# Performance work log

Hardware: AMD Instinct MI355X
Metric: run time of the kernel (lower is better)

## Reference

```python
import jax, jax.numpy as jnp
import numpy as np

N = 100000
E = 1600000
IN_C = 128
OUT_C = 64
ALPHA = 0.2  # LeakyReLU negative slope


def _xavier(key, shape, gain=1.414):
    fan_in, fan_out = shape[-2] if len(shape) > 1 else shape[-1], shape[-1]
    bound = gain * np.sqrt(6.0 / (shape[0] * 0 + (shape[-2] if len(shape) > 1 else 1) + shape[-1])) if False else gain * np.sqrt(6.0 / (sum(shape)))
    return jax.random.uniform(key, shape, jnp.float32, -bound, bound)


def setup_inputs() -> dict:
    key = jax.random.key(0)
    k_x, k_s, k_o, k_w, k_a = jax.random.split(key, 5)
    x = jax.random.normal(k_x, (N, IN_C), jnp.float32)
    # edge list with no self-loops (so remove_self_loops is a no-op)
    src = jax.random.randint(k_s, (E,), 0, N)
    off = jax.random.randint(k_o, (E,), 1, N)
    dst = (src + off) % N
    edge_index = jnp.stack([src, dst]).astype(jnp.int64)
    W = _xavier(k_w, (IN_C, OUT_C))
    a = _xavier(k_a, (1, 2 * OUT_C))
    return {"x": x, "W": W, "a": a, "edge_index": edge_index}


def reference(x, W, a, edge_index):
    h = x @ W                               # [N, D]
    n, d = h.shape
    loops = jnp.arange(n, dtype=edge_index.dtype)
    src = jnp.concatenate([edge_index[0], loops])   # add_self_loops
    dst = jnp.concatenate([edge_index[1], loops])
    # (cat(h[src], h[dst]) * a).sum(-1) == h[src]@a1 + h[dst]@a2
    a1, a2 = a[0, :d], a[0, d:]
    s = h @ a1                              # [N]
    t = h @ a2                              # [N]
    edge_e = jnp.exp(jax.nn.leaky_relu(s[src] + t[dst], negative_slope=ALPHA))  # [E+N]
    e_expsum = jax.ops.segment_sum(edge_e, src, num_segments=n)                  # [N]
    h_prime = jax.ops.segment_sum(edge_e[:, None] * h[dst], src, num_segments=n)  # [N, D]
    return h_prime / e_expsum[:, None]
```

## Files before the change

### kernel.cpp

```cpp
#include <hip/hip_runtime.h>
#include <math.h>

#define IN_C 128
#define OUT_C 64
#define ALPHA 0.2f

#define SCAN_BLOCK 256
#define SCAN_ITEMS 4
#define SCAN_TILE (SCAN_BLOCK * SCAN_ITEMS)

#define LDK 136

#define PA_EPT 16
#define PA_TILE (256 * PA_EPT)
#define BSH 9
#define NPB 512
#define MAXB 256

typedef __attribute__((ext_vector_type(8))) short short8;
typedef __attribute__((ext_vector_type(4))) float v4f;

__device__ __forceinline__ ushort f2b(float f) {
  unsigned u = __float_as_uint(f);
  u += 0x7fffu + ((u >> 16) & 1u);
  return (ushort)(u >> 16);
}
__device__ __forceinline__ float b2f(ushort h) {
  return __uint_as_float(((unsigned)h) << 16);
}

__global__ __launch_bounds__(256) void gemm_st_kernel(
    const float* __restrict__ x, const float* __restrict__ W,
    const float* __restrict__ a, ushort* __restrict__ hb,
    float* __restrict__ s, float* __restrict__ t, int n_nodes, int n_tiles) {
  __shared__ ushort xs[64 * LDK];
  __shared__ ushort ws[64 * LDK];

  const int tid = threadIdx.x;
  const int wave = tid >> 6;
  const int lane = tid & 63;
  const int li = lane & 15;
  const int quad = lane >> 4;

  for (int i = tid; i < IN_C * OUT_C; i += 256) {
    const int k = i >> 6;
    const int n = i & 63;
    ws[n * LDK + k] = f2b(W[i]);
  }
  __syncthreads();

  short8 bfrag[4][4];
#pragma unroll
  for (int ct = 0; ct < 4; ++ct)
#pragma unroll
    for (int kk = 0; kk < 4; ++kk)
      bfrag[ct][kk] =
          *(const short8*)&ws[(ct * 16 + li) * LDK + kk * 32 + quad * 8];

  float a1v[4], a2v[4];
#pragma unroll
  for (int ct = 0; ct < 4; ++ct) {
    a1v[ct] = a[ct * 16 + li];
    a2v[ct] = a[OUT_C + ct * 16 + li];
  }

  for (int tile = blockIdx.x; tile < n_tiles; tile += gridDim.x) {
    const int row0 = tile * 64;

    __syncthreads();
    for (int i = tid; i < 64 * (IN_C / 4); i += 256) {
      const int r = i >> 5;
      const int c4 = i & 31;
      int row = row0 + r;
      row = row < n_nodes ? row : n_nodes - 1;
      const float4 v = *(const float4*)&x[(size_t)row * IN_C + c4 * 4];
      uint2 p;
      p.x = (unsigned)f2b(v.x) | ((unsigned)f2b(v.y) << 16);
      p.y = (unsigned)f2b(v.z) | ((unsigned)f2b(v.w) << 16);
      *(uint2*)&xs[r * LDK + c4 * 4] = p;
    }
    __syncthreads();

    v4f acc[4];
#pragma unroll
    for (int ct = 0; ct < 4; ++ct) acc[ct] = (v4f){0.f, 0.f, 0.f, 0.f};

    const int rbase = wave * 16;
#pragma unroll
    for (int kk = 0; kk < 4; ++kk) {
      const short8 af =
          *(const short8*)&xs[(rbase + li) * LDK + kk * 32 + quad * 8];
#pragma unroll
      for (int ct = 0; ct < 4; ++ct)
        acc[ct] = __builtin_amdgcn_mfma_f32_16x16x32_bf16(af, bfrag[ct][kk],
                                                          acc[ct], 0, 0, 0);
    }

    const int growbase = row0 + rbase + quad * 4;
    float ps[4] = {0.f, 0.f, 0.f, 0.f};
    float pt[4] = {0.f, 0.f, 0.f, 0.f};
#pragma unroll
    for (int ct = 0; ct < 4; ++ct) {
#pragma unroll
      for (int r = 0; r < 4; ++r) {
        const float hv = acc[ct][r];
        ps[r] += hv * a1v[ct];
        pt[r] += hv * a2v[ct];
        const int grow = growbase + r;
        if (grow < n_nodes)
          hb[(size_t)grow * OUT_C + ct * 16 + li] = f2b(hv);
      }
    }
#pragma unroll
    for (int m = 1; m <= 8; m <<= 1) {
#pragma unroll
      for (int r = 0; r < 4; ++r) {
        ps[r] += __shfl_xor(ps[r], m, 64);
        pt[r] += __shfl_xor(pt[r], m, 64);
      }
    }
    if (li < 4) {
      const int grow = growbase + li;
      if (grow < n_nodes) {
        const float sv = li == 0 ? ps[0] : li == 1 ? ps[1] : li == 2 ? ps[2] : ps[3];
        const float tv = li == 0 ? pt[0] : li == 1 ? pt[1] : li == 2 ? pt[2] : pt[3];
        s[grow] = sv;
        t[grow] = tv;
      }
    }
  }
}

__global__ __launch_bounds__(256) void pa_count(const int* __restrict__ src,
                                                int* __restrict__ counts_tbl,
                                                int nblk_a, int E) {
  __shared__ int hist[MAXB];
  const int tid = threadIdx.x;
  hist[tid] = 0;
  __syncthreads();
  const int e0 = blockIdx.x * PA_TILE + tid * PA_EPT;
  if (e0 + PA_EPT <= E) {
#pragma unroll
    for (int i = 0; i < PA_EPT / 4; ++i) {
      const int4 v = *(const int4*)(src + e0 + i * 4);
      atomicAdd(&hist[v.x >> BSH], 1);
      atomicAdd(&hist[v.y >> BSH], 1);
      atomicAdd(&hist[v.z >> BSH], 1);
      atomicAdd(&hist[v.w >> BSH], 1);
    }
  } else {
    for (int e = e0; e < E; ++e) atomicAdd(&hist[src[e] >> BSH], 1);
  }
  __syncthreads();
  counts_tbl[(size_t)tid * nblk_a + blockIdx.x] = hist[tid];
}

__global__ __launch_bounds__(SCAN_BLOCK) void scan_partial(
    const int* __restrict__ cnt, int* __restrict__ block_sums, int n) {
  const int tid = threadIdx.x;
  const int base = blockIdx.x * SCAN_TILE + tid * SCAN_ITEMS;
  int s = 0;
#pragma unroll
  for (int i = 0; i < SCAN_ITEMS; ++i) {
    const int idx = base + i;
    if (idx < n) s += cnt[idx];
  }
  __shared__ int wsum[SCAN_BLOCK / 64];
#pragma unroll
  for (int off = 32; off; off >>= 1) s += __shfl_down(s, off, 64);
  if ((tid & 63) == 0) wsum[tid >> 6] = s;
  __syncthreads();
  if (tid == 0) {
    int tot = 0;
#pragma unroll
    for (int w = 0; w < SCAN_BLOCK / 64; ++w) tot += wsum[w];
    block_sums[blockIdx.x] = tot;
  }
}

__global__ __launch_bounds__(1024) void scan_blocksums(
    int* __restrict__ block_sums, int nb) {
  __shared__ int sh[1024];
  const int tid = threadIdx.x;
  const int v = (tid < nb) ? block_sums[tid] : 0;
  sh[tid] = v;
  __syncthreads();
  int val = v;
  for (int off = 1; off < 1024; off <<= 1) {
    const int other = (tid >= off) ? sh[tid - off] : 0;
    __syncthreads();
    val += other;
    sh[tid] = val;
    __syncthreads();
  }
  if (tid < nb) block_sums[tid] = val - v;
}

__global__ __launch_bounds__(SCAN_BLOCK) void scan_final_plain(
    const int* __restrict__ cnt, const int* __restrict__ block_sums,
    int* __restrict__ outv, int n) {
  __shared__ int tsum[SCAN_BLOCK];
  const int tid = threadIdx.x;
  const int base = blockIdx.x * SCAN_TILE + tid * SCAN_ITEMS;
  int local[SCAN_ITEMS];
  int s = 0;
#pragma unroll
  for (int i = 0; i < SCAN_ITEMS; ++i) {
    const int idx = base + i;
    local[i] = (idx < n) ? cnt[idx] : 0;
    s += local[i];
  }
  tsum[tid] = s;
  __syncthreads();
  int val = s;
  for (int off = 1; off < SCAN_BLOCK; off <<= 1) {
    const int other = (tid >= off) ? tsum[tid - off] : 0;
    __syncthreads();
    val += other;
    tsum[tid] = val;
    __syncthreads();
  }
  int prefix = block_sums[blockIdx.x] + (val - s);
#pragma unroll
  for (int i = 0; i < SCAN_ITEMS; ++i) {
    const int idx = base + i;
    if (idx < n) {
      outv[idx] = prefix;
      prefix += local[i];
    }
  }
}

__global__ __launch_bounds__(256) void pa_scatter(
    const int* __restrict__ src, const int* __restrict__ dst,
    const int* __restrict__ bases_tbl, int2* __restrict__ bpair, int nblk_a,
    int nbuck, int E) {
  __shared__ int cur[MAXB];
  const int tid = threadIdx.x;
  cur[tid] = (tid < nbuck) ? bases_tbl[(size_t)tid * nblk_a + blockIdx.x] : 0;
  __syncthreads();
  const int e0 = blockIdx.x * PA_TILE + tid * PA_EPT;
  if (e0 + PA_EPT <= E) {
#pragma unroll
    for (int i = 0; i < PA_EPT / 4; ++i) {
      const int4 sv = *(const int4*)(src + e0 + i * 4);
      const int4 dv = *(const int4*)(dst + e0 + i * 4);
      const int p0 = atomicAdd(&cur[sv.x >> BSH], 1);
      const int p1 = atomicAdd(&cur[sv.y >> BSH], 1);
      const int p2 = atomicAdd(&cur[sv.z >> BSH], 1);
      const int p3 = atomicAdd(&cur[sv.w >> BSH], 1);
      bpair[p0] = make_int2(sv.x, dv.x);
      bpair[p1] = make_int2(sv.y, dv.y);
      bpair[p2] = make_int2(sv.z, dv.z);
      bpair[p3] = make_int2(sv.w, dv.w);
    }
  } else {
    for (int e = e0; e < E; ++e) {
      const int sv = src[e];
      const int dv = dst[e];
      const int p = atomicAdd(&cur[sv >> BSH], 1);
      bpair[p] = make_int2(sv, dv);
    }
  }
}

__global__ __launch_bounds__(256) void pb_build(
    const int2* __restrict__ bpair, const int* __restrict__ bases_tbl,
    int* __restrict__ offs, int* __restrict__ dst_sorted, int n_nodes,
    int nblk_a, int nbuck, int E) {
  __shared__ int cnt[NPB];
  __shared__ int loffs[NPB];
  __shared__ int tsum[256];
  const int b = blockIdx.x;
  const int tid = threadIdx.x;
  const int bstart = bases_tbl[(size_t)b * nblk_a];
  const int bend = (b + 1 < nbuck) ? bases_tbl[(size_t)(b + 1) * nblk_a] : E;
  const int nbase = b << BSH;

  for (int i = tid; i < NPB; i += 256) cnt[i] = 0;
  __syncthreads();
  for (int e = bstart + tid; e < bend; e += 256)
    atomicAdd(&cnt[bpair[e].x - nbase], 1);
  __syncthreads();

  const int a0 = cnt[2 * tid];
  const int a1 = cnt[2 * tid + 1];
  const int tv = a0 + a1;
  tsum[tid] = tv;
  __syncthreads();
  int val = tv;
  for (int off = 1; off < 256; off <<= 1) {
    const int other = (tid >= off) ? tsum[tid - off] : 0;
    __syncthreads();
    val += other;
    tsum[tid] = val;
    __syncthreads();
  }
  const int pfx = val - tv;
  loffs[2 * tid] = pfx;
  loffs[2 * tid + 1] = pfx + a0;
  __syncthreads();

  for (int i = tid; i < NPB; i += 256) {
    const int node = nbase + i;
    const int gpos = bstart + loffs[i];
    if (node < n_nodes) offs[node] = gpos;
    cnt[i] = gpos;
  }
  if (b == 0 && tid == 0) offs[n_nodes] = E;
  __syncthreads();

  for (int e = bstart + tid; e < bend; e += 256) {
    const int2 pr = bpair[e];
    const int pos = atomicAdd(&cnt[pr.x - nbase], 1);
    dst_sorted[pos] = pr.y;
  }
}

__global__ __launch_bounds__(256) void aggregate_kernel(
    const int* __restrict__ offs, const int* __restrict__ dst_sorted,
    const uint* __restrict__ hbp, const float* __restrict__ s,
    const float* __restrict__ t, float* __restrict__ out, int n_nodes) {
  __shared__ int2 stage[4][64];
  const int wv = threadIdx.x >> 6;
  const int lane = threadIdx.x & 63;
  const int ch2 = lane & 31;
  const int half = lane >> 5;
  const int gwave = (blockIdx.x * blockDim.x + threadIdx.x) >> 6;
  const int waves_total = (gridDim.x * blockDim.x) >> 6;

  for (int u = gwave; u < n_nodes; u += waves_total) {
    const float su = s[u];
    const int beg = offs[u];
    const int end = offs[u + 1];

    float acc0 = 0.f, acc1 = 0.f, denom = 0.f;
    if (half == 0) {
      const float z0 = su + t[u];
      const float w0 = expf(z0 > 0.f ? z0 : ALPHA * z0);
      const uint p = hbp[(size_t)u * 32 + ch2];
      acc0 = w0 * __uint_as_float(p << 16);
      acc1 = w0 * __uint_as_float(p & 0xffff0000u);
      denom = w0;
    }

    for (int b = beg; b < end; b += 64) {
      const int rem = end - b;
      const int j = b + lane;
      const int idx = j < end ? j : end - 1;
      const int v = dst_sorted[idx];
      const float tv = t[v];
      const float z = su + tv;
      float w = expf(z > 0.f ? z : ALPHA * z);
      if (j >= end) w = 0.f;
      stage[wv][lane] = make_int2(v, __float_as_int(w));

      const int npad = min((rem + 15) & ~15, 64);
      for (int jj = 0; jj < npad; jj += 16) {
        int vj[8];
        float wj[8];
#pragma unroll
        for (int q = 0; q < 8; ++q) {
          const int2 evw = stage[wv][jj + 8 * half + q];
          vj[q] = evw.x;
          wj[q] = __int_as_float(evw.y);
        }
        uint p[8];
#pragma unroll
        for (int q = 0; q < 8; ++q) p[q] = hbp[(size_t)vj[q] * 32 + ch2];
#pragma unroll
        for (int q = 0; q < 8; ++q) {
          acc0 += wj[q] * __uint_as_float(p[q] << 16);
          acc1 += wj[q] * __uint_as_float(p[q] & 0xffff0000u);
          denom += wj[q];
        }
      }
    }
    acc0 += __shfl_xor(acc0, 32, 64);
    acc1 += __shfl_xor(acc1, 32, 64);
    denom += __shfl_xor(denom, 32, 64);
    if (half == 0) {
      float2 o;
      o.x = acc0 / denom;
      o.y = acc1 / denom;
      *(float2*)&out[(size_t)u * OUT_C + ch2 * 2] = o;
    }
  }
}

extern "C" void kernel_launch(void* const* d_in, const int* in_sizes, int n_in,
                              void* d_out, int out_size, void* d_ws,
                              size_t ws_size, hipStream_t stream) {
  const float* x = (const float*)d_in[0];
  const float* W = (const float*)d_in[1];
  const float* a = (const float*)d_in[2];
  const int* edge_index = (const int*)d_in[3];

  const int n_nodes = in_sizes[0] / IN_C;
  const int E = in_sizes[3] / 2;
  const int* src = edge_index;
  const int* dst = edge_index + E;

  float* out = (float*)d_out;

  const int nbuck = (n_nodes + NPB - 1) >> BSH;
  const int nblk_a = (E + PA_TILE - 1) / PA_TILE;
  const int tbl_n = nbuck * nblk_a;
  const int n_scan_blocks = (tbl_n + SCAN_TILE - 1) / SCAN_TILE;

  ushort* hb = (ushort*)d_ws;
  int2* bpair = (int2*)(hb + (size_t)n_nodes * OUT_C);
  float* s = (float*)(bpair + E);
  float* t = s + n_nodes;
  int* offs = (int*)(t + n_nodes);
  int* counts_tbl = offs + n_nodes + 1;
  int* bases_tbl = counts_tbl + (size_t)MAXB * nblk_a;
  int* block_sums = bases_tbl + (size_t)MAXB * nblk_a;
  int* dst_sorted = block_sums + 1024;

  {
    const int n_tiles = (n_nodes + 63) / 64;
    gemm_st_kernel<<<n_tiles, 256, 0, stream>>>(x, W, a, hb, s, t, n_nodes,
                                                n_tiles);
  }

  pa_count<<<nblk_a, 256, 0, stream>>>(src, counts_tbl, nblk_a, E);
  scan_partial<<<n_scan_blocks, SCAN_BLOCK, 0, stream>>>(counts_tbl,
                                                         block_sums, tbl_n);
  scan_blocksums<<<1, 1024, 0, stream>>>(block_sums, n_scan_blocks);
  scan_final_plain<<<n_scan_blocks, SCAN_BLOCK, 0, stream>>>(
      counts_tbl, block_sums, bases_tbl, tbl_n);
  pa_scatter<<<nblk_a, 256, 0, stream>>>(src, dst, bases_tbl, bpair, nblk_a,
                                         nbuck, E);
  pb_build<<<nbuck, 256, 0, stream>>>(bpair, bases_tbl, offs, dst_sorted,
                                      n_nodes, nblk_a, nbuck, E);

  {
    const int waves_per_block = 4;
    const int grid = (n_nodes + waves_per_block - 1) / waves_per_block;
    aggregate_kernel<<<grid, 256, 0, stream>>>(offs, dst_sorted, (const uint*)hb,
                                               s, t, out, n_nodes);
  }
}
```

Measured before the change: 193.4 us.

## Replace two-pass bucketed CSR build with global-atomic counting sort

Replaces the two-level bucket partition (block histograms, table scan, bucket scatter, per-bucket local sort) with a direct per-node global atomic histogram, a scan over nodes, and an atomic scatter into dst_sorted. This removes the intermediate int2 pair buffer and one full pass over the edges, and cuts the number of kernels. In exchange it relies on contended global atomics and random scattered writes, which may cost more than the LDS-local atomics it replaces. The order of edges within a node now depends on atomic ordering, so results are nondeterministic. A memset is added to clear the counts.

Result: slower. 363.8 us (+88.1%).

```diff
diff --git a/kernel.cpp b/kernel.cpp
--- a/kernel.cpp
+++ b/kernel.cpp
@@ -10,12 +10,6 @@
 #define SCAN_TILE (SCAN_BLOCK * SCAN_ITEMS)
 
 #define LDK 136
-
-#define PA_EPT 16
-#define PA_TILE (256 * PA_EPT)
-#define BSH 9
-#define NPB 512
-#define MAXB 256
 
 typedef __attribute__((ext_vector_type(8))) short short8;
 typedef __attribute__((ext_vector_type(4))) float v4f;
@@ -24,9 +18,6 @@
   unsigned u = __float_as_uint(f);
   u += 0x7fffu + ((u >> 16) & 1u);
   return (ushort)(u >> 16);
-}
-__device__ __forceinline__ float b2f(ushort h) {
-  return __uint_as_float(((unsigned)h) << 16);
 }
 
 __global__ __launch_bounds__(256) void gemm_st_kernel(
@@ -131,28 +122,19 @@
   }
 }
 
-__global__ __launch_bounds__(256) void pa_count(const int* __restrict__ src,
-                                                int* __restrict__ counts_tbl,
-                                                int nblk_a, int E) {
-  __shared__ int hist[MAXB];
-  const int tid = threadIdx.x;
-  hist[tid] = 0;
-  __syncthreads();
-  const int e0 = blockIdx.x * PA_TILE + tid * PA_EPT;
-  if (e0 + PA_EPT <= E) {
-#pragma unroll
-    for (int i = 0; i < PA_EPT / 4; ++i) {
-      const int4 v = *(const int4*)(src + e0 + i * 4);
-      atomicAdd(&hist[v.x >> BSH], 1);
-      atomicAdd(&hist[v.y >> BSH], 1);
-      atomicAdd(&hist[v.z >> BSH], 1);
-      atomicAdd(&hist[v.w >> BSH], 1);
-    }
+__global__ __launch_bounds__(256) void count_atomic(const int* __restrict__ src,
+                                                    int* __restrict__ cnt,
+                                                    int E) {
+  const int e0 = (blockIdx.x * 256 + threadIdx.x) * 4;
+  if (e0 + 4 <= E) {
+    const int4 v = *(const int4*)(src + e0);
+    atomicAdd(&cnt[v.x], 1);
+    atomicAdd(&cnt[v.y], 1);
+    atomicAdd(&cnt[v.z], 1);
+    atomicAdd(&cnt[v.w], 1);
   } else {
-    for (int e = e0; e < E; ++e) atomicAdd(&hist[src[e] >> BSH], 1);
-  }
-  __syncthreads();
-  counts_tbl[(size_t)tid * nblk_a + blockIdx.x] = hist[tid];
+    for (int e = e0; e < E; ++e) atomicAdd(&cnt[src[e]], 1);
+  }
 }
 
 __global__ __launch_bounds__(SCAN_BLOCK) void scan_partial(
@@ -196,9 +178,9 @@
   if (tid < nb) block_sums[tid] = val - v;
 }
 
-__global__ __launch_bounds__(SCAN_BLOCK) void scan_final_plain(
+__global__ __launch_bounds__(SCAN_BLOCK) void scan_final_dual(
     const int* __restrict__ cnt, const int* __restrict__ block_sums,
-    int* __restrict__ outv, int n) {
+    int* __restrict__ offs, int* __restrict__ cur, int n, int total) {
   __shared__ int tsum[SCAN_BLOCK];
   const int tid = threadIdx.x;
   const int base = blockIdx.x * SCAN_TILE + tid * SCAN_ITEMS;
@@ -225,95 +207,32 @@
   for (int i = 0; i < SCAN_ITEMS; ++i) {
     const int idx = base + i;
     if (idx < n) {
-      outv[idx] = prefix;
+      offs[idx] = prefix;
+      cur[idx] = prefix;
       prefix += local[i];
     }
   }
-}
-
-__global__ __launch_bounds__(256) void pa_scatter(
+  if (blockIdx.x == 0 && tid == 0) offs[n] = total;
+}
+
+__global__ __launch_bounds__(256) void scatter_atomic(
     const int* __restrict__ src, const int* __restrict__ dst,
-    const int* __restrict__ bases_tbl, int2* __restrict__ bpair, int nblk_a,
-    int nbuck, int E) {
-  __shared__ int cur[MAXB];
-  const int tid = threadIdx.x;
-  cur[tid] = (tid < nbuck) ? bases_tbl[(size_t)tid * nblk_a + blockIdx.x] : 0;
-  __syncthreads();
-  const int e0 = blockIdx.x * PA_TILE + tid * PA_EPT;
-  if (e0 + PA_EPT <= E) {
-#pragma unroll
-    for (int i = 0; i < PA_EPT / 4; ++i) {
-      const int4 sv = *(const int4*)(src + e0 + i * 4);
-      const int4 dv = *(const int4*)(dst + e0 + i * 4);
-      const int p0 = atomicAdd(&cur[sv.x >> BSH], 1);
-      const int p1 = atomicAdd(&cur[sv.y >> BSH], 1);
-      const int p2 = atomicAdd(&cur[sv.z >> BSH], 1);
-      const int p3 = atomicAdd(&cur[sv.w >> BSH], 1);
-      bpair[p0] = make_int2(sv.x, dv.x);
-      bpair[p1] = make_int2(sv.y, dv.y);
-      bpair[p2] = make_int2(sv.z, dv.z);
-      bpair[p3] = make_int2(sv.w, dv.w);
-    }
+    int* __restrict__ cur, int* __restrict__ dst_sorted, int E) {
+  const int e0 = (blockIdx.x * 256 + threadIdx.x) * 4;
+  if (e0 + 4 <= E) {
+    const int4 sv = *(const int4*)(src + e0);
+    const int4 dv = *(const int4*)(dst + e0);
+    const int p0 = atomicAdd(&cur[sv.x], 1);
+    const int p1 = atomicAdd(&cur[sv.y], 1);
+    const int p2 = atomicAdd(&cur[sv.z], 1);
+    const int p3 = atomicAdd(&cur[sv.w], 1);
+    dst_sorted[p0] = dv.x;
+    dst_sorted[p1] = dv.y;
+    dst_sorted[p2] = dv.z;
+    dst_sorted[p3] = dv.w;
   } else {
-    for (int e = e0; e < E; ++e) {
-      const int sv = src[e];
-      const int dv = dst[e];
-      const int p = atomicAdd(&cur[sv >> BSH], 1);
-      bpair[p] = make_int2(sv, dv);
-    }
-  }
-}
-
-__global__ __launch_bounds__(256) void pb_build(
-    const int2* __restrict__ bpair, const int* __restrict__ bases_tbl,
-    int* __restrict__ offs, int* __restrict__ dst_sorted, int n_nodes,
-    int nblk_a, int nbuck, int E) {
-  __shared__ int cnt[NPB];
-  __shared__ int loffs[NPB];
-  __shared__ int tsum[256];
-  const int b = blockIdx.x;
-  const int tid = threadIdx.x;
-  const int bstart = bases_tbl[(size_t)b * nblk_a];
-  const int bend = (b + 1 < nbuck) ? bases_tbl[(size_t)(b + 1) * nblk_a] : E;
-  const int nbase = b << BSH;
-
-  for (int i = tid; i < NPB; i += 256) cnt[i] = 0;
-  __syncthreads();
-  for (int e = bstart + tid; e < bend; e += 256)
-    atomicAdd(&cnt[bpair[e].x - nbase], 1);
-  __syncthreads();
-
-  const int a0 = cnt[2 * tid];
-  const int a1 = cnt[2 * tid + 1];
-  const int tv = a0 + a1;
-  tsum[tid] = tv;
-  __syncthreads();
-  int val = tv;
-  for (int off = 1; off < 256; off <<= 1) {
-    const int other = (tid >= off) ? tsum[tid - off] : 0;
-    __syncthreads();
-    val += other;
-    tsum[tid] = val;
-    __syncthreads();
-  }
-  const int pfx = val - tv;
-  loffs[2 * tid] = pfx;
-  loffs[2 * tid + 1] = pfx + a0;
-  __syncthreads();
-
-  for (int i = tid; i < NPB; i += 256) {
-    const int node = nbase + i;
-    const int gpos = bstart + loffs[i];
-    if (node < n_nodes) offs[node] = gpos;
-    cnt[i] = gpos;
-  }
-  if (b == 0 && tid == 0) offs[n_nodes] = E;
-  __syncthreads();
-
-  for (int e = bstart + tid; e < bend; e += 256) {
-    const int2 pr = bpair[e];
-    const int pos = atomicAdd(&cnt[pr.x - nbase], 1);
-    dst_sorted[pos] = pr.y;
+    for (int e = e0; e < E; ++e)
+      dst_sorted[atomicAdd(&cur[src[e]], 1)] = dst[e];
   }
 }
 
@@ -403,20 +322,19 @@
 
   float* out = (float*)d_out;
 
-  const int nbuck = (n_nodes + NPB - 1) >> BSH;
-  const int nblk_a = (E + PA_TILE - 1) / PA_TILE;
-  const int tbl_n = nbuck * nblk_a;
-  const int n_scan_blocks = (tbl_n + SCAN_TILE - 1) / SCAN_TILE;
-
   ushort* hb = (ushort*)d_ws;
-  int2* bpair = (int2*)(hb + (size_t)n_nodes * OUT_C);
-  float* s = (float*)(bpair + E);
+  float* s = (float*)(hb + (size_t)n_nodes * OUT_C);
   float* t = s + n_nodes;
   int* offs = (int*)(t + n_nodes);
-  int* counts_tbl = offs + n_nodes + 1;
-  int* bases_tbl = counts_tbl + (size_t)MAXB * nblk_a;
-  int* block_sums = bases_tbl + (size_t)MAXB * nblk_a;
+  int* cnt = offs + n_nodes + 1;
+  int* cur = cnt + n_nodes;
+  int* block_sums = cur + n_nodes;
   int* dst_sorted = block_sums + 1024;
+
+  const int nblk_e = (E + 1023) / 1024;
+  const int n_scan_blocks = (n_nodes + SCAN_TILE - 1) / SCAN_TILE;
+
+  hipMemsetAsync(cnt, 0, sizeof(int) * (size_t)n_nodes, stream);
 
   {
     const int n_tiles = (n_nodes + 63) / 64;
@@ -424,16 +342,13 @@
                                                 n_tiles);
   }
 
-  pa_count<<<nblk_a, 256, 0, stream>>>(src, counts_tbl, nblk_a, E);
-  scan_partial<<<n_scan_blocks, SCAN_BLOCK, 0, stream>>>(counts_tbl,
-                                                         block_sums, tbl_n);
+  count_atomic<<<nblk_e, 256, 0, stream>>>(src, cnt, E);
+  scan_partial<<<n_scan_blocks, SCAN_BLOCK, 0, stream>>>(cnt, block_sums,
+                                                         n_nodes);
   scan_blocksums<<<1, 1024, 0, stream>>>(block_sums, n_scan_blocks);
-  scan_final_plain<<<n_scan_blocks, SCAN_BLOCK, 0, stream>>>(
-      counts_tbl, block_sums, bases_tbl, tbl_n);
-  pa_scatter<<<nblk_a, 256, 0, stream>>>(src, dst, bases_tbl, bpair, nblk_a,
-                                         nbuck, E);
-  pb_build<<<nbuck, 256, 0, stream>>>(bpair, bases_tbl, offs, dst_sorted,
-                                      n_nodes, nblk_a, nbuck, E);
+  scan_final_dual<<<n_scan_blocks, SCAN_BLOCK, 0, stream>>>(
+      cnt, block_sums, offs, cur, n_nodes, E);
+  scatter_atomic<<<nblk_e, 256, 0, stream>>>(src, dst, cur, dst_sorted, E);
 
   {
     const int waves_per_block = 4;
```

## Precompute edge weights in CSR build and restructure aggregation lanes

Applied to the files above, without the earlier changes.

The CSR build kernel now computes each edge's attention weight (exp of leaky-relu of s[src]+t[dst]) and stores it with the destination in an int2 adjacency array. Self-loops are inserted directly into the CSR. The aggregation kernel drops its shared-memory staging and t[] gathers: each group of 16 lanes reads 4 channels per row and processes 4 edges per iteration. Bucket size is halved (256 nodes, up to 512 buckets) to fit one thread per node in the prefix scan. In exchange the adjacency array is twice as large to write and read, and the smaller buckets enlarge the count/scan tables.

Measured after the change: 205.4 us. 6.2% more time.

```diff
diff --git a/kernel.cpp b/kernel.cpp
--- a/kernel.cpp
+++ b/kernel.cpp
@@ -13,9 +13,9 @@
 
 #define PA_EPT 16
 #define PA_TILE (256 * PA_EPT)
-#define BSH 9
-#define NPB 512
-#define MAXB 256
+#define BSH 8
+#define NPB 256
+#define MAXB 512
 
 typedef __attribute__((ext_vector_type(8))) short short8;
 typedef __attribute__((ext_vector_type(4))) float v4f;
@@ -24,9 +24,6 @@
   unsigned u = __float_as_uint(f);
   u += 0x7fffu + ((u >> 16) & 1u);
   return (ushort)(u >> 16);
-}
-__device__ __forceinline__ float b2f(ushort h) {
-  return __uint_as_float(((unsigned)h) << 16);
 }
 
 __global__ __launch_bounds__(256) void gemm_st_kernel(
@@ -133,10 +130,11 @@
 
 __global__ __launch_bounds__(256) void pa_count(const int* __restrict__ src,
                                                 int* __restrict__ counts_tbl,
-                                                int nblk_a, int E) {
+                                                int nblk_a, int nbuck, int E) {
   __shared__ int hist[MAXB];
   const int tid = threadIdx.x;
   hist[tid] = 0;
+  hist[tid + 256] = 0;
   __syncthreads();
   const int e0 = blockIdx.x * PA_TILE + tid * PA_EPT;
   if (e0 + PA_EPT <= E) {
@@ -152,7 +150,8 @@
     for (int e = e0; e < E; ++e) atomicAdd(&hist[src[e] >> BSH], 1);
   }
   __syncthreads();
-  counts_tbl[(size_t)tid * nblk_a + blockIdx.x] = hist[tid];
+  for (int i = tid; i < nbuck; i += 256)
+    counts_tbl[(size_t)i * nblk_a + blockIdx.x] = hist[i];
 }
 
 __global__ __launch_bounds__(SCAN_BLOCK) void scan_partial(
@@ -237,7 +236,8 @@
     int nbuck, int E) {
   __shared__ int cur[MAXB];
   const int tid = threadIdx.x;
-  cur[tid] = (tid < nbuck) ? bases_tbl[(size_t)tid * nblk_a + blockIdx.x] : 0;
+  for (int i = tid; i < MAXB; i += 256)
+    cur[i] = (i < nbuck) ? bases_tbl[(size_t)i * nblk_a + blockIdx.x] : 0;
   __syncthreads();
   const int e0 = blockIdx.x * PA_TILE + tid * PA_EPT;
   if (e0 + PA_EPT <= E) {
@@ -266,124 +266,112 @@
 
 __global__ __launch_bounds__(256) void pb_build(
     const int2* __restrict__ bpair, const int* __restrict__ bases_tbl,
-    int* __restrict__ offs, int* __restrict__ dst_sorted, int n_nodes,
-    int nblk_a, int nbuck, int E) {
+    const float* __restrict__ s, const float* __restrict__ t,
+    int* __restrict__ offs, int2* __restrict__ adj, int n_nodes, int nblk_a,
+    int nbuck, int E) {
   __shared__ int cnt[NPB];
-  __shared__ int loffs[NPB];
-  __shared__ int tsum[256];
+  __shared__ int tsum[NPB];
   const int b = blockIdx.x;
   const int tid = threadIdx.x;
   const int bstart = bases_tbl[(size_t)b * nblk_a];
   const int bend = (b + 1 < nbuck) ? bases_tbl[(size_t)(b + 1) * nblk_a] : E;
   const int nbase = b << BSH;
-
-  for (int i = tid; i < NPB; i += 256) cnt[i] = 0;
+  const int node = nbase + tid;
+
+  cnt[tid] = (node < n_nodes) ? 1 : 0;
   __syncthreads();
   for (int e = bstart + tid; e < bend; e += 256)
     atomicAdd(&cnt[bpair[e].x - nbase], 1);
   __syncthreads();
 
-  const int a0 = cnt[2 * tid];
-  const int a1 = cnt[2 * tid + 1];
-  const int tv = a0 + a1;
-  tsum[tid] = tv;
-  __syncthreads();
-  int val = tv;
-  for (int off = 1; off < 256; off <<= 1) {
+  const int myc = cnt[tid];
+  tsum[tid] = myc;
+  __syncthreads();
+  int val = myc;
+  for (int off = 1; off < NPB; off <<= 1) {
     const int other = (tid >= off) ? tsum[tid - off] : 0;
     __syncthreads();
     val += other;
     tsum[tid] = val;
     __syncthreads();
   }
-  const int pfx = val - tv;
-  loffs[2 * tid] = pfx;
-  loffs[2 * tid + 1] = pfx + a0;
-  __syncthreads();
-
-  for (int i = tid; i < NPB; i += 256) {
-    const int node = nbase + i;
-    const int gpos = bstart + loffs[i];
-    if (node < n_nodes) offs[node] = gpos;
-    cnt[i] = gpos;
-  }
-  if (b == 0 && tid == 0) offs[n_nodes] = E;
+  const int gpos = bstart + b * NPB + (val - myc);
+
+  if (node < n_nodes) {
+    offs[node] = gpos;
+    const float z0 = s[node] + t[node];
+    const float w0 = expf(z0 > 0.f ? z0 : ALPHA * z0);
+    adj[gpos] = make_int2(node, __float_as_int(w0));
+  }
+  cnt[tid] = gpos + 1;
+  if (b == 0 && tid == 0) offs[n_nodes] = E + n_nodes;
   __syncthreads();
 
   for (int e = bstart + tid; e < bend; e += 256) {
     const int2 pr = bpair[e];
     const int pos = atomicAdd(&cnt[pr.x - nbase], 1);
-    dst_sorted[pos] = pr.y;
+    const float z = s[pr.x] + t[pr.y];
+    const float w = expf(z > 0.f ? z : ALPHA * z);
+    adj[pos] = make_int2(pr.y, __float_as_int(w));
   }
 }
 
 __global__ __launch_bounds__(256) void aggregate_kernel(
-    const int* __restrict__ offs, const int* __restrict__ dst_sorted,
-    const uint* __restrict__ hbp, const float* __restrict__ s,
-    const float* __restrict__ t, float* __restrict__ out, int n_nodes) {
-  __shared__ int2 stage[4][64];
-  const int wv = threadIdx.x >> 6;
+    const int* __restrict__ offs, const int2* __restrict__ adj,
+    const uint* __restrict__ hbp, float* __restrict__ out, int n_nodes) {
   const int lane = threadIdx.x & 63;
-  const int ch2 = lane & 31;
-  const int half = lane >> 5;
+  const int g = lane >> 4;
+  const int il = lane & 15;
   const int gwave = (blockIdx.x * blockDim.x + threadIdx.x) >> 6;
   const int waves_total = (gridDim.x * blockDim.x) >> 6;
 
   for (int u = gwave; u < n_nodes; u += waves_total) {
-    const float su = s[u];
     const int beg = offs[u];
     const int end = offs[u + 1];
 
-    float acc0 = 0.f, acc1 = 0.f, denom = 0.f;
-    if (half == 0) {
-      const float z0 = su + t[u];
-      const float w0 = expf(z0 > 0.f ? z0 : ALPHA * z0);
-      const uint p = hbp[(size_t)u * 32 + ch2];
-      acc0 = w0 * __uint_as_float(p << 16);
-      acc1 = w0 * __uint_as_float(p & 0xffff0000u);
-      denom = w0;
-    }
-
-    for (int b = beg; b < end; b += 64) {
-      const int rem = end - b;
-      const int j = b + lane;
-      const int idx = j < end ? j : end - 1;
-      const int v = dst_sorted[idx];
-      const float tv = t[v];
-      const float z = su + tv;
-      float w = expf(z > 0.f ? z : ALPHA * z);
-      if (j >= end) w = 0.f;
-      stage[wv][lane] = make_int2(v, __float_as_int(w));
-
-      const int npad = min((rem + 15) & ~15, 64);
-      for (int jj = 0; jj < npad; jj += 16) {
-        int vj[8];
-        float wj[8];
-#pragma unroll
-        for (int q = 0; q < 8; ++q) {
-          const int2 evw = stage[wv][jj + 8 * half + q];
-          vj[q] = evw.x;
-          wj[q] = __int_as_float(evw.y);
-        }
-        uint p[8];
-#pragma unroll
-        for (int q = 0; q < 8; ++q) p[q] = hbp[(size_t)vj[q] * 32 + ch2];
-#pragma unroll
-        for (int q = 0; q < 8; ++q) {
-          acc0 += wj[q] * __uint_as_float(p[q] << 16);
-          acc1 += wj[q] * __uint_as_float(p[q] & 0xffff0000u);
-          denom += wj[q];
-        }
+    float acc0 = 0.f, acc1 = 0.f, acc2 = 0.f, acc3 = 0.f, denom = 0.f;
+
+    for (int b = beg; b < end; b += 16) {
+      int2 e[4];
+#pragma unroll
+      for (int c = 0; c < 4; ++c) {
+        const int j = b + c * 4 + g;
+        e[c] = adj[j < end ? j : beg];
+        if (j >= end) e[c].y = 0;
       }
-    }
+      uint2 p[4];
+#pragma unroll
+      for (int c = 0; c < 4; ++c)
+        p[c] = *(const uint2*)(hbp + (size_t)e[c].x * 32 + il * 2);
+#pragma unroll
+      for (int c = 0; c < 4; ++c) {
+        const float w = __int_as_float(e[c].y);
+        acc0 += w * __uint_as_float(p[c].x << 16);
+        acc1 += w * __uint_as_float(p[c].x & 0xffff0000u);
+        acc2 += w * __uint_as_float(p[c].y << 16);
+        acc3 += w * __uint_as_float(p[c].y & 0xffff0000u);
+        denom += w;
+      }
+    }
+    acc0 += __shfl_xor(acc0, 16, 64);
+    acc1 += __shfl_xor(acc1, 16, 64);
+    acc2 += __shfl_xor(acc2, 16, 64);
+    acc3 += __shfl_xor(acc3, 16, 64);
+    denom += __shfl_xor(denom, 16, 64);
     acc0 += __shfl_xor(acc0, 32, 64);
     acc1 += __shfl_xor(acc1, 32, 64);
+    acc2 += __shfl_xor(acc2, 32, 64);
+    acc3 += __shfl_xor(acc3, 32, 64);
     denom += __shfl_xor(denom, 32, 64);
-    if (half == 0) {
-      float2 o;
-      o.x = acc0 / denom;
-      o.y = acc1 / denom;
-      *(float2*)&out[(size_t)u * OUT_C + ch2 * 2] = o;
+
+    if (g == 0) {
+      const float inv = 1.f / denom;
+      float4 o;
+      o.x = acc0 * inv;
+      o.y = acc1 * inv;
+      o.z = acc2 * inv;
+      o.w = acc3 * inv;
+      *(float4*)&out[(size_t)u * OUT_C + il * 4] = o;
     }
   }
 }
@@ -410,13 +398,13 @@
 
   ushort* hb = (ushort*)d_ws;
   int2* bpair = (int2*)(hb + (size_t)n_nodes * OUT_C);
-  float* s = (float*)(bpair + E);
+  int2* adj = bpair + E;
+  float* s = (float*)(adj + (size_t)E + (size_t)nbuck * NPB);
   float* t = s + n_nodes;
   int* offs = (int*)(t + n_nodes);
   int* counts_tbl = offs + n_nodes + 1;
-  int* bases_tbl = counts_tbl + (size_t)MAXB * nblk_a;
-  int* block_sums = bases_tbl + (size_t)MAXB * nblk_a;
-  int* dst_sorted = block_sums + 1024;
+  int* bases_tbl = counts_tbl + tbl_n;
+  int* block_sums = bases_tbl + tbl_n;
 
   {
     const int n_tiles = (n_nodes + 63) / 64;
@@ -424,7 +412,7 @@
                                                 n_tiles);
   }
 
-  pa_count<<<nblk_a, 256, 0, stream>>>(src, counts_tbl, nblk_a, E);
+  pa_count<<<nblk_a, 256, 0, stream>>>(src, counts_tbl, nblk_a, nbuck, E);
   scan_partial<<<n_scan_blocks, SCAN_BLOCK, 0, stream>>>(counts_tbl,
                                                          block_sums, tbl_n);
   scan_blocksums<<<1, 1024, 0, stream>>>(block_sums, n_scan_blocks);
@@ -432,13 +420,13 @@
       counts_tbl, block_sums, bases_tbl, tbl_n);
   pa_scatter<<<nblk_a, 256, 0, stream>>>(src, dst, bases_tbl, bpair, nblk_a,
                                          nbuck, E);
-  pb_build<<<nbuck, 256, 0, stream>>>(bpair, bases_tbl, offs, dst_sorted,
+  pb_build<<<nbuck, 256, 0, stream>>>(bpair, bases_tbl, s, t, offs, adj,
                                       n_nodes, nblk_a, nbuck, E);
 
   {
     const int waves_per_block = 4;
     const int grid = (n_nodes + waves_per_block - 1) / waves_per_block;
-    aggregate_kernel<<<grid, 256, 0, stream>>>(offs, dst_sorted, (const uint*)hb,
-                                               s, t, out, n_nodes);
-  }
-}
+    aggregate_kernel<<<grid, 256, 0, stream>>>(offs, adj, (const uint*)hb, out,
+                                               n_nodes);
+  }
+}
```
